# Performance work log

Measured on AMD Instinct MI355X. Metric: run time of the kernel, lower is better.

Reference implementation:

```python
import jax, jax.numpy as jnp
import numpy as np

D_MODEL = 1024
HEADS = 16
DK = D_MODEL // HEADS
B, S = 2, 2048


def setup_inputs() -> dict:
    key = jax.random.key(0)
    ks = jax.random.split(key, 9)
    s = 0.02
    return {
        "Q": jax.random.normal(ks[0], (B, S, D_MODEL), jnp.float32),
        "K": jax.random.normal(ks[1], (B, S, D_MODEL), jnp.float32),
        "V": jax.random.normal(ks[2], (B, S, D_MODEL), jnp.float32),
        "mask": jnp.ones((B, 1, S), jnp.int32),
        "Wq": jax.random.normal(ks[3], (D_MODEL, D_MODEL), jnp.float32) * s,
        "Wk": jax.random.normal(ks[4], (D_MODEL, D_MODEL), jnp.float32) * s,
        "Wv": jax.random.normal(ks[5], (D_MODEL, D_MODEL), jnp.float32) * s,
        "Wo": jax.random.normal(ks[6], (D_MODEL, D_MODEL), jnp.float32) * s,
        "ln_gamma": jnp.ones((D_MODEL,), jnp.float32),
        "ln_beta": jnp.zeros((D_MODEL,), jnp.float32),
    }


def _layer_norm(x, gamma, beta, eps=1e-5):
    mu = jnp.mean(x, axis=-1, keepdims=True)
    var = jnp.mean(jnp.square(x - mu), axis=-1, keepdims=True)
    return (x - mu) * jax.lax.rsqrt(var + eps) * gamma + beta


def reference(Q, K, V, mask, Wq, Wk, Wv, Wo, ln_gamma, ln_beta):
    # torch Linear(no bias): y = x @ W.T
    def split_heads(x):  # [B,S,D] -> [B,H,S,dk]
        return x.reshape(B, -1, HEADS, DK).transpose(0, 2, 1, 3)

    q = split_heads(Q @ Wq.T)
    k = split_heads(K @ Wk.T)
    v = split_heads(V @ Wv.T)

    # scores: [B,H,Sq,Sk]
    scores = jnp.einsum("bhqd,bhkd->bhqk", q, k) / np.sqrt(DK).astype(np.float32)
    m = mask[:, None, :, :]  # [B,1,1,S] broadcast over heads and queries
    scores = jnp.where(m == 0, -jnp.inf, scores)
    attn = jax.nn.softmax(scores, axis=-1)  # dropout is identity in eval
    out = jnp.einsum("bhqk,bhkd->bhqd", attn, v)
    out = out.transpose(0, 2, 1, 3).reshape(B, -1, D_MODEL)
    out = out @ Wo.T
    return _layer_norm(out + Q, ln_gamma, ln_beta)
```

## Files before the change

### kernel.cpp

```cpp
#include <hip/hip_runtime.h>
#include <hip/hip_bf16.h>
#include <stdint.h>

#define NB 2
#define NS 2048
#define ND 1024
#define NH 16
#define NDK 64
#define NM (NB*NS)

using bf16x8 = __attribute__((ext_vector_type(8))) short;
using f32x4  = __attribute__((ext_vector_type(4))) float;
using f32x16 = __attribute__((ext_vector_type(16))) float;
using u32x4  = __attribute__((ext_vector_type(4))) unsigned;

__device__ __forceinline__ unsigned short f2bf(float f){
  unsigned u = __float_as_uint(f);
  u += 0x7fffu + ((u>>16)&1u);
  return (unsigned short)(u>>16);
}

__device__ __forceinline__ void gload_lds16(const void* g, void* l){
  __builtin_amdgcn_global_load_lds((const __attribute__((address_space(1))) void*)g,
                                   (__attribute__((address_space(3))) void*)l, 16, 0, 0);
}

__device__ __forceinline__ float fexp2(float x){
#if __has_builtin(__builtin_amdgcn_exp2f)
  return __builtin_amdgcn_exp2f(x);
#else
  return __expf(x * 0.69314718056f);
#endif
}

__device__ __forceinline__ unsigned cvtpk_bf16(float lo, float hi){
  unsigned r;
  asm("v_cvt_pk_bf16_f32 %0, %1, %2" : "=v"(r) : "v"(lo), "v"(hi));
  return r;
}

__device__ __forceinline__ void swap32(unsigned &a, unsigned &b){
#if __has_builtin(__builtin_amdgcn_permlane32_swap)
  auto rr = __builtin_amdgcn_permlane32_swap((int)a, (int)b, false, false);
  a = (unsigned)rr[0]; b = (unsigned)rr[1];
#else
  const bool lo = (threadIdx.x & 32) == 0;
  unsigned sa = (unsigned)__shfl_xor((int)a, 32, 64);
  unsigned sb = (unsigned)__shfl_xor((int)b, 32, 64);
  unsigned na = lo ? a : sb;
  unsigned nb = lo ? sa : b;
  a = na; b = nb;
#endif
}

__device__ __forceinline__ f32x16 mfma32(bf16x8 a, bf16x8 b, f32x16 c){
  return __builtin_amdgcn_mfma_f32_32x32x16_bf16(a, b, c, 0, 0, 0);
}

__global__ __launch_bounds__(256) void prep_k(const float* __restrict__ Q, const float* __restrict__ K,
                                              const float* __restrict__ V, const float* __restrict__ Wq,
                                              const float* __restrict__ Wk, const float* __restrict__ Wv,
                                              const float* __restrict__ Wo,
                                              unsigned short* __restrict__ Xbf,
                                              unsigned short* __restrict__ Wbf){
  const int bid = blockIdx.x;
  const float* src; unsigned short* dst; int i;
  if (bid < 12288){
    const int which = bid >> 12;
    src = (which==0) ? Q : (which==1) ? K : V;
    dst = Xbf + ((size_t)which << 22);
    i = (bid & 4095)*256 + threadIdx.x;
  } else {
    const int which = (bid - 12288) >> 10;
    src = (which==0) ? Wq : (which==1) ? Wk : (which==2) ? Wv : Wo;
    dst = Wbf + ((size_t)which << 20);
    i = ((bid - 12288) & 1023)*256 + threadIdx.x;
  }
  float4 v = ((const float4*)src)[i];
  ushort4 o;
  o.x = f2bf(v.x); o.y = f2bf(v.y); o.z = f2bf(v.z); o.w = f2bf(v.w);
  ((ushort4*)dst)[i] = o;
}

__global__ __launch_bounds__(256) void gemm_qkv(const short* __restrict__ Xbf, const short* __restrict__ Wbf,
                                                unsigned short* __restrict__ qh, unsigned short* __restrict__ kh,
                                                unsigned short* __restrict__ vT){
  __shared__ short lsA[2][4096];
  __shared__ short lsB[2][4096];
  const int tid = threadIdx.x;
  const int hw = blockIdx.x;
  const int logical = (hw & 7)*96 + (hw >> 3);
  const int z = logical >> 8, rem = logical & 255;
  const int my = rem >> 3, nx = rem & 7;
  const short* A = Xbf + (size_t)z*NM*ND;
  const short* W = Wbf + (size_t)z*ND*ND;
  unsigned short* out = (z==0) ? qh : (z==1) ? kh : vT;
  const int mode = (z==2) ? 1 : 0;
  const int m0 = my*128, n0 = nx*128;

  const short* gA = A + (size_t)m0*1024;
  const short* gB = W + (size_t)n0*1024;
  const int srow = tid>>2;
  const int scol = ((tid&3)*8) ^ (((srow>>1)&3)<<3);
  const int w = tid>>6, lane = tid&63, lr = lane&15, lk = lane>>4;
  const int wm = w>>1, wn = w&1;

  f32x4 acc[4][4];
  #pragma unroll
  for (int i=0;i<4;++i)
    #pragma unroll
    for (int j=0;j<4;++j) acc[i][j] = (f32x4){0.f,0.f,0.f,0.f};

  #pragma unroll
  for (int r=0;r<2;++r){
    gload_lds16(gA + (size_t)(r*64+srow)*1024 + scol, &lsA[0][(r*256+tid)*8]);
    gload_lds16(gB + (size_t)(r*64+srow)*1024 + scol, &lsB[0][(r*256+tid)*8]);
  }
  int cur = 0;
  for (int ks=0; ks<32; ++ks){
    __syncthreads();
    if (ks+1 < 32){
      const int k0 = (ks+1)*32;
      #pragma unroll
      for (int r=0;r<2;++r){
        gload_lds16(gA + (size_t)(r*64+srow)*1024 + k0 + scol, &lsA[cur^1][(r*256+tid)*8]);
        gload_lds16(gB + (size_t)(r*64+srow)*1024 + k0 + scol, &lsB[cur^1][(r*256+tid)*8]);
      }
    }
    bf16x8 af[4], bfr[4];
    const char* Ab = (const char*)&lsA[cur][0];
    const char* Bb = (const char*)&lsB[cur][0];
    #pragma unroll
    for (int i=0;i<4;++i){
      const int ra = wm*64 + i*16 + lr;
      const int rb = wn*64 + i*16 + lr;
      af[i]  = *(const bf16x8*)(Ab + ra*64 + ((lk*16) ^ (((ra>>1)&3)<<4)));
      bfr[i] = *(const bf16x8*)(Bb + rb*64 + ((lk*16) ^ (((rb>>1)&3)<<4)));
    }
    #pragma unroll
    for (int i=0;i<4;++i)
      #pragma unroll
      for (int j=0;j<4;++j)
        acc[i][j] = __builtin_amdgcn_mfma_f32_16x16x32_bf16(af[i], bfr[j], acc[i][j], 0,0,0);
    cur ^= 1;
  }
  #pragma unroll
  for (int i=0;i<4;++i)
    #pragma unroll
    for (int j=0;j<4;++j)
      #pragma unroll
      for (int r=0;r<4;++r){
        const int m = m0 + wm*64 + i*16 + lk*4 + r;
        const int n = n0 + wn*64 + j*16 + lr;
        const float v = acc[i][j][r];
        const int b = m>>11, s = m&2047, h = n>>6, dk = n&63;
        size_t addr;
        if (mode == 0) addr = (((size_t)(b*NH+h))*NS + s)*NDK + dk;
        else           addr = (((size_t)(b*NH+h))*NDK + dk)*NS + s;
        out[addr] = f2bf(v);
      }
}

__global__ __launch_bounds__(256) void gemm_out(const short* __restrict__ Attn, const short* __restrict__ Wo,
                                                const float* __restrict__ Qin, float* __restrict__ proj){
  __shared__ short lsA[2][4096];
  __shared__ short lsB[2][4096];
  const int tid = threadIdx.x;
  const int hw = blockIdx.x;
  const int logical = (hw & 7)*32 + (hw >> 3);
  const int my = logical >> 3, nx = logical & 7;
  const int m0 = my*128, n0 = nx*128;
  const short* gA = Attn + (size_t)m0*1024;
  const short* gB = Wo + (size_t)n0*1024;
  const int srow = tid>>2;
  const int scol = ((tid&3)*8) ^ (((srow>>1)&3)<<3);
  const int w = tid>>6, lane = tid&63, lr = lane&15, lk = lane>>4;
  const int wm = w>>1, wn = w&1;

  f32x4 acc[4][4];
  #pragma unroll
  for (int i=0;i<4;++i)
    #pragma unroll
    for (int j=0;j<4;++j) acc[i][j] = (f32x4){0.f,0.f,0.f,0.f};

  #pragma unroll
  for (int r=0;r<2;++r){
    gload_lds16(gA + (size_t)(r*64+srow)*1024 + scol, &lsA[0][(r*256+tid)*8]);
    gload_lds16(gB + (size_t)(r*64+srow)*1024 + scol, &lsB[0][(r*256+tid)*8]);
  }
  int cur = 0;
  for (int ks=0; ks<32; ++ks){
    __syncthreads();
    if (ks+1 < 32){
      const int k0 = (ks+1)*32;
      #pragma unroll
      for (int r=0;r<2;++r){
        gload_lds16(gA + (size_t)(r*64+srow)*1024 + k0 + scol, &lsA[cur^1][(r*256+tid)*8]);
        gload_lds16(gB + (size_t)(r*64+srow)*1024 + k0 + scol, &lsB[cur^1][(r*256+tid)*8]);
      }
    }
    bf16x8 af[4], bfr[4];
    const char* Ab = (const char*)&lsA[cur][0];
    const char* Bb = (const char*)&lsB[cur][0];
    #pragma unroll
    for (int i=0;i<4;++i){
      const int ra = wm*64 + i*16 + lr;
      const int rb = wn*64 + i*16 + lr;
      af[i]  = *(const bf16x8*)(Ab + ra*64 + ((lk*16) ^ (((ra>>1)&3)<<4)));
      bfr[i] = *(const bf16x8*)(Bb + rb*64 + ((lk*16) ^ (((rb>>1)&3)<<4)));
    }
    #pragma unroll
    for (int i=0;i<4;++i)
      #pragma unroll
      for (int j=0;j<4;++j)
        acc[i][j] = __builtin_amdgcn_mfma_f32_16x16x32_bf16(af[i], bfr[j], acc[i][j], 0,0,0);
    cur ^= 1;
  }
  #pragma unroll
  for (int i=0;i<4;++i)
    #pragma unroll
    for (int j=0;j<4;++j)
      #pragma unroll
      for (int r=0;r<4;++r){
        const int m = m0 + wm*64 + i*16 + lk*4 + r;
        const int n = n0 + wn*64 + j*16 + lr;
        proj[(size_t)m*1024 + n] = acc[i][j][r] + Qin[(size_t)m*1024 + n];
      }
}

__global__ __launch_bounds__(256) void attn_k(const short* __restrict__ qh, const short* __restrict__ kh,
                                              const short* __restrict__ vT, const int* __restrict__ mask,
                                              unsigned short* __restrict__ attn){
  __shared__ char sb[32768];
  const int hw = blockIdx.x;
  const int logical = (hw & 7)*64 + (hw >> 3);
  const int qb = logical & 15, h = (logical>>4)&15, b = logical>>8;
  const int tid = threadIdx.x, w = tid>>6, lane = tid&63;
  const int ql = lane & 31, hi = lane>>5;
  const int bh = b*NH + h;
  const int q0 = qb*128 + w*32;
  const float C2 = 0.18033688f;

  const int D = tid*16;
  const int strow = D>>7;
  const int scb = (D&127) ^ ((strow&7)<<4);
  const char* ksrcb = (const char*)kh + (size_t)bh*NS*NDK*2;
  const char* vsrcb = (const char*)vT + (size_t)bh*NDK*NS*2;

  const short* qrow = qh + ((size_t)bh*NS + q0 + ql)*NDK + hi*8;
  bf16x8 qf[4];
  #pragma unroll
  for (int kp=0;kp<4;++kp) qf[kp] = *(const bf16x8*)(qrow + kp*16);

  const int* mrow = mask + b*NS;

  #pragma unroll
  for (int p=0;p<2;++p){
    gload_lds16(ksrcb + (size_t)(p*32+strow)*128 + scb,            sb + p*4096 + D);
    gload_lds16(vsrcb + (size_t)(p*32+strow)*4096 + scb,           sb + 16384 + p*4096 + D);
  }

  f32x16 o0, o1;
  #pragma unroll
  for (int r=0;r<16;++r){ o0[r]=0.f; o1[r]=0.f; }
  float mrun = -1e30f, lrun = 0.f;

  const int swz = (ql&7)<<4;

  for (int t=0; t<32; ++t){
    const int kv0 = t*64;
    const int buf = (t&1)*8192;
    __syncthreads();
    if (t+1 < 32){
      const int nbuf = ((t+1)&1)*8192;
      const int kvn = kv0 + 64;
      #pragma unroll
      for (int p=0;p<2;++p){
        gload_lds16(ksrcb + (size_t)(kvn + p*32 + strow)*128 + scb,          sb + nbuf + p*4096 + D);
        gload_lds16(vsrcb + (size_t)(p*32+strow)*4096 + kvn*2 + scb,         sb + 16384 + nbuf + p*4096 + D);
      }
    }
    const unsigned long long bal = __ballot(mrow[kv0 + lane] != 0);
    const unsigned mw0 = (unsigned)bal, mw1 = (unsigned)(bal>>32);
    const bool allm = (~bal) == 0ull;

    const char* kb = sb + buf;
    const char* vb = sb + 16384 + buf;

    bf16x8 kf[8];
    #pragma unroll
    for (int kvh=0;kvh<2;++kvh)
      #pragma unroll
      for (int kp=0;kp<4;++kp)
        kf[kvh*4+kp] = *(const bf16x8*)(kb + (((kvh*32+ql)*128 + kp*32 + hi*16) ^ swz));

    f32x16 s0, s1;
    #pragma unroll
    for (int r=0;r<16;++r){ s0[r]=0.f; s1[r]=0.f; }
    __builtin_amdgcn_s_setprio(1);
    #pragma unroll
    for (int kp=0;kp<4;++kp){
      s0 = mfma32(kf[kp],   qf[kp], s0);
      s1 = mfma32(kf[4+kp], qf[kp], s1);
    }
    __builtin_amdgcn_s_setprio(0);

    float t16[16];
    #pragma unroll
    for (int r=0;r<16;++r) t16[r] = fmaxf(s0[r], s1[r]);
    #pragma unroll
    for (int st=8; st>=1; st>>=1)
      #pragma unroll
      for (int r=0;r<st;++r) t16[r] = fmaxf(t16[r], t16[r+st]);
    const float tm = fmaxf(t16[0], __shfl_xor(t16[0], 32, 64));

    if (!__all(tm - mrun <= 32.f)){
      const float mnew = fmaxf(mrun, tm);
      const float fac  = fexp2((mrun - mnew)*C2);
      mrun = mnew;
      #pragma unroll
      for (int r=0;r<16;++r){ o0[r]*=fac; o1[r]*=fac; }
      lrun *= fac;
    }
    const float nb = mrun*C2;

    bf16x8 vf[8];
    #pragma unroll
    for (int dh=0;dh<2;++dh)
      #pragma unroll
      for (int c=0;c<4;++c)
        vf[dh*4+c] = *(const bf16x8*)(vb + (((dh*32+ql)*128 + c*32 + hi*16) ^ swz));

    float psum = 0.f;
    #pragma unroll
    for (int kvh=0; kvh<2; ++kvh){
      const f32x16& ss = kvh ? s1 : s0;
      const unsigned mw = kvh ? mw1 : mw0;
      unsigned pwd[8];
      float ps0 = 0.f, ps1 = 0.f;
      #pragma unroll
      for (int i=0;i<8;++i){
        const int bp0 = ((2*i)&3) + 8*((2*i)>>2);
        float p0 = fexp2(ss[2*i]*C2   - nb);
        float p1 = fexp2(ss[2*i+1]*C2 - nb);
        if (!allm){
          p0 = ((mw >> (bp0     + 4*hi)) & 1u) ? p0 : 0.f;
          p1 = ((mw >> (bp0 + 1 + 4*hi)) & 1u) ? p1 : 0.f;
        }
        ps0 += p0; ps1 += p1;
        pwd[i] = cvtpk_bf16(p0, p1);
      }
      psum += ps0 + ps1;
      swap32(pwd[0], pwd[2]);
      swap32(pwd[1], pwd[3]);
      swap32(pwd[4], pwd[6]);
      swap32(pwd[5], pwd[7]);
      u32x4 c0w = {pwd[0], pwd[1], pwd[2], pwd[3]};
      u32x4 c1w = {pwd[4], pwd[5], pwd[6], pwd[7]};
      bf16x8 pf0 = __builtin_bit_cast(bf16x8, c0w);
      bf16x8 pf1 = __builtin_bit_cast(bf16x8, c1w);
      __builtin_amdgcn_s_setprio(1);
      o0 = mfma32(vf[2*kvh],       pf0, o0);
      o1 = mfma32(vf[4 + 2*kvh],   pf0, o1);
      o0 = mfma32(vf[2*kvh + 1],   pf1, o0);
      o1 = mfma32(vf[4 + 2*kvh+1], pf1, o1);
      __builtin_amdgcn_s_setprio(0);
    }
    psum += __shfl_xor(psum, 32, 64);
    lrun += psum;
  }

  __syncthreads();
  const float inv = 1.f / lrun;
  char* ep = sb + w*4096;
  #pragma unroll
  for (int dh=0; dh<2; ++dh){
    const f32x16& oo = dh ? o1 : o0;
    #pragma unroll
    for (int i=0;i<8;++i){
      const int d0 = ((2*i)&3) + 8*((2*i)>>2) + 4*hi + dh*32;
      const unsigned pk = cvtpk_bf16(oo[2*i]*inv, oo[2*i+1]*inv);
      *(unsigned*)(ep + (((ql*128) + d0*2) ^ ((ql&7)<<4))) = pk;
    }
  }
  asm volatile("s_waitcnt lgkmcnt(0)" ::: "memory");
  #pragma unroll
  for (int seg=0; seg<4; ++seg){
    const int qq = seg*8 + (lane>>3), dc = (lane&7)*8;
    bf16x8 vv = *(const bf16x8*)(ep + (((qq*128) + dc*2) ^ ((qq&7)<<4)));
    *(bf16x8*)(attn + ((size_t)b*NS + q0 + qq)*ND + h*NDK + dc) = vv;
  }
}

__global__ __launch_bounds__(256) void ln_k(const float* __restrict__ proj,
                                            const float* __restrict__ gamma, const float* __restrict__ beta,
                                            float* __restrict__ out){
  const int row = blockIdx.x*4 + (threadIdx.x>>6);
  const int lane = threadIdx.x & 63;
  const float4* pp = (const float4*)(proj + (size_t)row*ND);
  float4 x[4];
  float sum = 0.f;
  #pragma unroll
  for (int i=0;i<4;++i){
    x[i] = pp[lane + i*64];
    sum += x[i].x + x[i].y + x[i].z + x[i].w;
  }
  #pragma unroll
  for (int off=32; off>=1; off>>=1) sum += __shfl_xor(sum, off, 64);
  const float mu = sum * (1.f/1024.f);
  float vs = 0.f;
  #pragma unroll
  for (int i=0;i<4;++i){
    float d0=x[i].x-mu, d1=x[i].y-mu, d2=x[i].z-mu, d3=x[i].w-mu;
    vs += d0*d0 + d1*d1 + d2*d2 + d3*d3;
  }
  #pragma unroll
  for (int off=32; off>=1; off>>=1) vs += __shfl_xor(vs, off, 64);
  const float rstd = rsqrtf(vs*(1.f/1024.f) + 1e-5f);
  #pragma unroll
  for (int i=0;i<4;++i){
    const float4 g  = ((const float4*)gamma)[lane + i*64];
    const float4 be = ((const float4*)beta)[lane + i*64];
    float4 y;
    y.x = (x[i].x-mu)*rstd*g.x + be.x;
    y.y = (x[i].y-mu)*rstd*g.y + be.y;
    y.z = (x[i].z-mu)*rstd*g.z + be.z;
    y.w = (x[i].w-mu)*rstd*g.w + be.w;
    ((float4*)(out + (size_t)row*ND))[lane + i*64] = y;
  }
}

extern "C" void kernel_launch(void* const* d_in, const int* in_sizes, int n_in,
                              void* d_out, int out_size, void* d_ws, size_t ws_size,
                              hipStream_t stream){
  const float* Q    = (const float*)d_in[0];
  const float* K    = (const float*)d_in[1];
  const float* V    = (const float*)d_in[2];
  const int*   mask = (const int*)  d_in[3];
  const float* Wq   = (const float*)d_in[4];
  const float* Wk   = (const float*)d_in[5];
  const float* Wv   = (const float*)d_in[6];
  const float* Wo   = (const float*)d_in[7];
  const float* gam  = (const float*)d_in[8];
  const float* bet  = (const float*)d_in[9];
  float* out = (float*)d_out;
  char* ws = (char*)d_ws;

  unsigned short* Wbf  = (unsigned short*)(ws);
  unsigned short* Xbf  = (unsigned short*)(ws + (size_t)(8u<<20));
  unsigned short* qhp  = (unsigned short*)(ws + (size_t)(32u<<20));
  unsigned short* khp  = (unsigned short*)(ws + (size_t)(40u<<20));
  unsigned short* vTp  = (unsigned short*)(ws + (size_t)(48u<<20));
  unsigned short* attb = (unsigned short*)(ws + (size_t)(56u<<20));
  float* proj  = (float*)(ws + (size_t)(8u<<20));

  prep_k<<<16384,256,0,stream>>>(Q, K, V, Wq, Wk, Wv, Wo, Xbf, Wbf);

  gemm_qkv<<<768,256,0,stream>>>((const short*)Xbf, (const short*)Wbf, qhp, khp, vTp);

  attn_k<<<512,256,0,stream>>>((const short*)qhp, (const short*)khp, (const short*)vTp, mask, attb);

  gemm_out<<<256,256,0,stream>>>((const short*)attb, (const short*)(Wbf + (3u<<20)), Q, proj);

  ln_k<<<1024,256,0,stream>>>(proj, gam, bet, out);
}
```

Baseline: 164.4 us.

## Split attention along the key dimension into two halves with a combine kernel

The attention kernel now splits each (batch, head, query-block) over two halves of the key sequence, doubling the grid from 512 to 1024 blocks. Each half writes unnormalized bf16 partial outputs plus its running max and sum to workspace. A new combine kernel merges the halves with log-sum-exp rescaling and writes the normalized head-interleaved output. The aim is better fill of the GPU's compute units, at the cost of an extra launch, extra global traffic, and an additional bf16 rounding of the partial results.

Result: slower. 173.8 us (+5.7%).

```diff
diff --git a/kernel.cpp b/kernel.cpp
--- a/kernel.cpp
+++ b/kernel.cpp
@@ -18,6 +18,10 @@
   unsigned u = __float_as_uint(f);
   u += 0x7fffu + ((u>>16)&1u);
   return (unsigned short)(u>>16);
+}
+
+__device__ __forceinline__ float bf2f(short v){
+  return __uint_as_float(((unsigned)(unsigned short)v) << 16);
 }
 
 __device__ __forceinline__ void gload_lds16(const void* g, void* l){
@@ -230,34 +234,36 @@
 
 __global__ __launch_bounds__(256) void attn_k(const short* __restrict__ qh, const short* __restrict__ kh,
                                               const short* __restrict__ vT, const int* __restrict__ mask,
-                                              unsigned short* __restrict__ attn){
+                                              unsigned short* __restrict__ po, float* __restrict__ mp,
+                                              float* __restrict__ lp){
   __shared__ char sb[32768];
   const int hw = blockIdx.x;
-  const int logical = (hw & 7)*64 + (hw >> 3);
-  const int qb = logical & 15, h = (logical>>4)&15, b = logical>>8;
+  const int logical = (hw & 7)*128 + (hw >> 3);
+  const int half = logical & 1, qb = (logical>>1) & 15, h = (logical>>5) & 15, b = logical>>9;
   const int tid = threadIdx.x, w = tid>>6, lane = tid&63;
   const int ql = lane & 31, hi = lane>>5;
   const int bh = b*NH + h;
+  const int u = bh*2 + half;
   const int q0 = qb*128 + w*32;
   const float C2 = 0.18033688f;
 
   const int D = tid*16;
   const int strow = D>>7;
   const int scb = (D&127) ^ ((strow&7)<<4);
-  const char* ksrcb = (const char*)kh + (size_t)bh*NS*NDK*2;
-  const char* vsrcb = (const char*)vT + (size_t)bh*NDK*NS*2;
+  const char* ksrcb = (const char*)kh + (size_t)bh*NS*NDK*2 + (size_t)half*1024*128;
+  const char* vsrcb = (const char*)vT + (size_t)bh*NDK*NS*2 + (size_t)half*1024*2;
 
   const short* qrow = qh + ((size_t)bh*NS + q0 + ql)*NDK + hi*8;
   bf16x8 qf[4];
   #pragma unroll
   for (int kp=0;kp<4;++kp) qf[kp] = *(const bf16x8*)(qrow + kp*16);
 
-  const int* mrow = mask + b*NS;
+  const int* mrow = mask + b*NS + half*1024;
 
   #pragma unroll
   for (int p=0;p<2;++p){
-    gload_lds16(ksrcb + (size_t)(p*32+strow)*128 + scb,            sb + p*4096 + D);
-    gload_lds16(vsrcb + (size_t)(p*32+strow)*4096 + scb,           sb + 16384 + p*4096 + D);
+    gload_lds16(ksrcb + (size_t)(p*32+strow)*128 + scb,   sb + p*4096 + D);
+    gload_lds16(vsrcb + (size_t)(p*32+strow)*4096 + scb,  sb + 16384 + p*4096 + D);
   }
 
   f32x16 o0, o1;
@@ -267,17 +273,17 @@
 
   const int swz = (ql&7)<<4;
 
-  for (int t=0; t<32; ++t){
+  for (int t=0; t<16; ++t){
     const int kv0 = t*64;
     const int buf = (t&1)*8192;
     __syncthreads();
-    if (t+1 < 32){
+    if (t+1 < 16){
       const int nbuf = ((t+1)&1)*8192;
       const int kvn = kv0 + 64;
       #pragma unroll
       for (int p=0;p<2;++p){
-        gload_lds16(ksrcb + (size_t)(kvn + p*32 + strow)*128 + scb,          sb + nbuf + p*4096 + D);
-        gload_lds16(vsrcb + (size_t)(p*32+strow)*4096 + kvn*2 + scb,         sb + 16384 + nbuf + p*4096 + D);
+        gload_lds16(ksrcb + (size_t)(kvn + p*32 + strow)*128 + scb,   sb + nbuf + p*4096 + D);
+        gload_lds16(vsrcb + (size_t)(p*32+strow)*4096 + kvn*2 + scb,  sb + 16384 + nbuf + p*4096 + D);
       }
     }
     const unsigned long long bal = __ballot(mrow[kv0 + lane] != 0);
@@ -371,7 +377,6 @@
   }
 
   __syncthreads();
-  const float inv = 1.f / lrun;
   char* ep = sb + w*4096;
   #pragma unroll
   for (int dh=0; dh<2; ++dh){
@@ -379,17 +384,47 @@
     #pragma unroll
     for (int i=0;i<8;++i){
       const int d0 = ((2*i)&3) + 8*((2*i)>>2) + 4*hi + dh*32;
-      const unsigned pk = cvtpk_bf16(oo[2*i]*inv, oo[2*i+1]*inv);
+      const unsigned pk = cvtpk_bf16(oo[2*i], oo[2*i+1]);
       *(unsigned*)(ep + (((ql*128) + d0*2) ^ ((ql&7)<<4))) = pk;
     }
   }
   asm volatile("s_waitcnt lgkmcnt(0)" ::: "memory");
+  unsigned short* pobase = po + (size_t)u*NS*NDK;
   #pragma unroll
   for (int seg=0; seg<4; ++seg){
     const int qq = seg*8 + (lane>>3), dc = (lane&7)*8;
     bf16x8 vv = *(const bf16x8*)(ep + (((qq*128) + dc*2) ^ ((qq&7)<<4)));
-    *(bf16x8*)(attn + ((size_t)b*NS + q0 + qq)*ND + h*NDK + dc) = vv;
-  }
+    *(bf16x8*)(pobase + (size_t)(q0 + qq)*NDK + dc) = vv;
+  }
+  if (hi == 0){
+    mp[(size_t)u*NS + q0 + ql] = mrun;
+    lp[(size_t)u*NS + q0 + ql] = lrun;
+  }
+}
+
+__global__ __launch_bounds__(256) void combine_k(const unsigned short* __restrict__ po,
+                                                 const float* __restrict__ mp, const float* __restrict__ lp,
+                                                 unsigned short* __restrict__ attb){
+  const int idx = blockIdx.x*256 + threadIdx.x;
+  const int d8 = idx & 7, q = (idx>>3) & 2047, bh = idx>>14;
+  const float C2 = 0.18033688f;
+  const float m0 = mp[(size_t)(bh*2+0)*NS + q], m1 = mp[(size_t)(bh*2+1)*NS + q];
+  const float l0 = lp[(size_t)(bh*2+0)*NS + q], l1 = lp[(size_t)(bh*2+1)*NS + q];
+  const float mf = fmaxf(m0, m1);
+  const float f0 = fexp2((m0-mf)*C2), f1 = fexp2((m1-mf)*C2);
+  const float inv = 1.f / (l0*f0 + l1*f1);
+  const float s0 = f0*inv, s1 = f1*inv;
+  const bf16x8 a0 = *(const bf16x8*)(po + ((size_t)(bh*2+0)*NS + q)*NDK + d8*8);
+  const bf16x8 a1 = *(const bf16x8*)(po + ((size_t)(bh*2+1)*NS + q)*NDK + d8*8);
+  u32x4 ow;
+  #pragma unroll
+  for (int j=0;j<4;++j){
+    const float x0 = bf2f(a0[2*j])*s0   + bf2f(a1[2*j])*s1;
+    const float x1 = bf2f(a0[2*j+1])*s0 + bf2f(a1[2*j+1])*s1;
+    ow[j] = cvtpk_bf16(x0, x1);
+  }
+  const int b = bh>>4, h = bh&15;
+  *(u32x4*)(attb + ((size_t)b*NS + q)*ND + h*NDK + d8*8) = ow;
 }
 
 __global__ __launch_bounds__(256) void ln_k(const float* __restrict__ proj,
@@ -452,13 +487,19 @@
   unsigned short* khp  = (unsigned short*)(ws + (size_t)(40u<<20));
   unsigned short* vTp  = (unsigned short*)(ws + (size_t)(48u<<20));
   unsigned short* attb = (unsigned short*)(ws + (size_t)(56u<<20));
+  unsigned short* po   = (unsigned short*)(ws + (size_t)(8u<<20));
+  float* mp    = (float*)(ws + (size_t)(24u<<20));
+  float* lp    = (float*)(ws + (size_t)(24u<<20) + (1u<<19));
   float* proj  = (float*)(ws + (size_t)(8u<<20));
 
   prep_k<<<16384,256,0,stream>>>(Q, K, V, Wq, Wk, Wv, Wo, Xbf, Wbf);
 
   gemm_qkv<<<768,256,0,stream>>>((const short*)Xbf, (const short*)Wbf, qhp, khp, vTp);
 
-  attn_k<<<512,256,0,stream>>>((const short*)qhp, (const short*)khp, (const short*)vTp, mask, attb);
+  attn_k<<<1024,256,0,stream>>>((const short*)qhp, (const short*)khp, (const short*)vTp, mask,
+                                po, mp, lp);
+
+  combine_k<<<2048,256,0,stream>>>(po, mp, lp, attb);
 
   gemm_out<<<256,256,0,stream>>>((const short*)attb, (const short*)(Wbf + (3u<<20)), Q, proj);
 
```
